# Kernel tuning notes

Measured on AMD Instinct MI355X. Metric: run time of the kernel, lower is better.

## Reference

```python
import jax, jax.numpy as jnp
import numpy as np

D_MODEL = 512
NUM_HEADS = 8
D_FF = 2048
SEQ = 2048
BATCH = 2
EPS = 1e-5


def _linear(x, W, b):
    # x: [S,B,D_in], W: [D_out, D_in] (torch convention), b: [D_out]
    return jnp.einsum('sbd,ed->sbe', x, W) + b


def _layer_norm(x, g, b):
    mu = jnp.mean(x, axis=-1, keepdims=True)
    var = jnp.var(x, axis=-1, keepdims=True)
    return (x - mu) * jax.lax.rsqrt(var + EPS) * g + b


def _mha(q_in, k_in, v_in, W, b, mask4d, num_heads):
    # q_in: [Sq,B,D], k_in/v_in: [Sk,B,D]; W: [4,D,D], b: [4,D]
    Sq, B, D = q_in.shape
    Sk = k_in.shape[0]
    dk = D // num_heads
    q = _linear(q_in, W[0], b[0]).reshape(Sq, B, num_heads, dk).transpose(1, 2, 0, 3)
    k = _linear(k_in, W[1], b[1]).reshape(Sk, B, num_heads, dk).transpose(1, 2, 0, 3)
    v = _linear(v_in, W[2], b[2]).reshape(Sk, B, num_heads, dk).transpose(1, 2, 0, 3)
    scores = jnp.einsum('bhqd,bhkd->bhqk', q, k) / jnp.sqrt(jnp.asarray(dk, q.dtype))
    scores = jnp.where(mask4d, -jnp.inf, scores)
    p = jax.nn.softmax(scores, axis=-1)  # dropout p=0 -> identity
    o = jnp.einsum('bhqk,bhkd->bhqd', p, v)  # [B,H,Sq,dk]
    o = o.transpose(2, 0, 1, 3).reshape(Sq, B, D)
    return _linear(o, W[3], b[3])


def setup_inputs() -> dict:
    key = jax.random.key(0)
    ks = jax.random.split(key, 12)
    scale = 1.0 / np.sqrt(D_MODEL)
    inp = {
        'x': jax.random.normal(ks[0], (SEQ, BATCH, D_MODEL), jnp.float32),
        'memory': jax.random.normal(ks[1], (SEQ, BATCH, D_MODEL), jnp.float32),
        # causal mask: True = masked (strictly upper triangular)
        'tgt_mask': jnp.triu(jnp.ones((SEQ, SEQ), dtype=bool), k=1),
        # per-batch key padding mask for cross attention
        'memory_mask': jax.random.randint(ks[2], (BATCH, SEQ), 0, 2) > 0,
        'sa_W': jax.random.normal(ks[3], (4, D_MODEL, D_MODEL), jnp.float32) * scale,
        'sa_b': jnp.zeros((4, D_MODEL), jnp.float32),
        'ca_W': jax.random.normal(ks[4], (4, D_MODEL, D_MODEL), jnp.float32) * scale,
        'ca_b': jnp.zeros((4, D_MODEL), jnp.float32),
        'w1': jax.random.normal(ks[5], (D_FF, D_MODEL), jnp.float32) * scale,
        'b1': jnp.zeros((D_FF,), jnp.float32),
        'w2': jax.random.normal(ks[6], (D_MODEL, D_FF), jnp.float32) * (1.0 / np.sqrt(D_FF)),
        'b2': jnp.zeros((D_MODEL,), jnp.float32),
        'ln_g': jnp.ones((3, D_MODEL), jnp.float32),
        'ln_b': jnp.zeros((3, D_MODEL), jnp.float32),
    }
    return inp


def reference(x, memory, tgt_mask, memory_mask, sa_W, sa_b, ca_W, ca_b,
              w1, b1, w2, b2, ln_g, ln_b):
    # self-attention block (pre-norm, residual)
    nx = _layer_norm(x, ln_g[0], ln_b[0])
    sa = _mha(nx, nx, nx, sa_W, sa_b, tgt_mask[None, None], NUM_HEADS)
    x = x + sa
    # cross-attention block
    nx = _layer_norm(x, ln_g[1], ln_b[1])
    ca = _mha(nx, memory, memory, ca_W, ca_b, memory_mask[:, None, None, :], NUM_HEADS)
    x = x + ca
    # FFN block
    nx = _layer_norm(x, ln_g[2], ln_b[2])
    ff = _linear(jax.nn.relu(_linear(nx, w1, b1)), w2, b2)
    return x + ff
```

## Files before the change

kernel.cpp:

```cpp
#include <hip/hip_runtime.h>

#define S_LEN 2048
#define BATCH_N 2
#define DM 512
#define H_N 8
#define DK_N 64
#define FF_N 2048
#define M_TOK (S_LEN*BATCH_N)
#define QSZ (BATCH_N*H_N*S_LEN*DK_N)

typedef __attribute__((ext_vector_type(8))) short short8;
typedef __attribute__((ext_vector_type(4))) float f32x4;
typedef __attribute__((ext_vector_type(16))) float f32x16;
typedef __attribute__((ext_vector_type(4))) unsigned uint4v;

__device__ __forceinline__ unsigned short f2b(float f) {
  union { float f; unsigned u; } v; v.f = f;
  unsigned r = v.u + 0x7FFFu + ((v.u >> 16) & 1u);
  return (unsigned short)(r >> 16);
}
__device__ __forceinline__ float b2f(unsigned short u) {
  union { unsigned u; float f; } v; v.u = ((unsigned)u) << 16; return v.f;
}

__device__ __forceinline__ void gl_lds16(const void* g, void* l) {
  __builtin_amdgcn_global_load_lds(
      (__attribute__((address_space(1))) unsigned int*)(unsigned long long)g,
      (__attribute__((address_space(3))) unsigned int*)(unsigned int)(unsigned long long)l,
      16, 0, 0);
}

__global__ void cast_kernel(const float* __restrict__ src,
                            unsigned short* __restrict__ dst, int n) {
  int i = (blockIdx.x * blockDim.x + threadIdx.x) * 4;
  if (i >= n) return;
  float4 v = *(const float4*)(src + i);
  ushort4 o; o.x = f2b(v.x); o.y = f2b(v.y); o.z = f2b(v.z); o.w = f2b(v.w);
  *(ushort4*)(dst + i) = o;
}

__global__ void maskpack(const int* __restrict__ mm, unsigned long long* __restrict__ bm) {
  int t = threadIdx.x;
  int b = t >> 5, kt = t & 31;
  unsigned long long m = 0ull;
  for (int j = 0; j < 64; j++)
    m |= (unsigned long long)(mm[b*S_LEN + kt*64 + j] != 0) << j;
  bm[b*32 + kt] = m;
}

__global__ __launch_bounds__(128) void ln_kernel(const float* __restrict__ in,
                                                 const float* __restrict__ g,
                                                 const float* __restrict__ b,
                                                 unsigned short* __restrict__ out) {
  int row = blockIdx.x, t = threadIdx.x;
  float4 v = ((const float4*)(in + (size_t)row * DM))[t];
  float s  = v.x + v.y + v.z + v.w;
  float ss = v.x*v.x + v.y*v.y + v.z*v.z + v.w*v.w;
  #pragma unroll
  for (int off = 32; off >= 1; off >>= 1) {
    s  += __shfl_xor(s,  off);
    ss += __shfl_xor(ss, off);
  }
  __shared__ float sh[4];
  if ((t & 63) == 0) { sh[(t>>6)*2] = s; sh[(t>>6)*2+1] = ss; }
  __syncthreads();
  s = sh[0] + sh[2]; ss = sh[1] + sh[3];
  float mean = s * (1.f/512.f);
  float inv  = rsqrtf(ss * (1.f/512.f) - mean*mean + 1e-5f);
  float4 gv = ((const float4*)g)[t];
  float4 bv = ((const float4*)b)[t];
  ushort4 o;
  o.x = f2b((v.x-mean)*inv*gv.x + bv.x);
  o.y = f2b((v.y-mean)*inv*gv.y + bv.y);
  o.z = f2b((v.z-mean)*inv*gv.z + bv.z);
  o.w = f2b((v.w-mean)*inv*gv.w + bv.w);
  ((ushort4*)out)[(size_t)row*128 + t] = o;
}

template<int RELU, int OUTMODE, int RESID>
__global__ __launch_bounds__(256) void gemm_bt(
    const unsigned short* __restrict__ A, const unsigned short* __restrict__ W,
    const float* __restrict__ bias, const float* __restrict__ resid,
    float* __restrict__ Cf, unsigned short* __restrict__ Cb,
    int M, int N, int K)
{
  __shared__ unsigned short As[64*40];
  __shared__ unsigned short Bs[64*40];
  int tid = threadIdx.x;
  int lane = tid & 63, w = tid >> 6;
  int wr = w >> 1, wc = w & 1;
  int bm = blockIdx.y * 64, bn = blockIdx.x * 64;
  f32x4 acc[2][2] = {};
  int lrow = tid >> 2;
  int lcg  = (tid & 3) * 8;
  const size_t aoff = (size_t)(bm + lrow) * K + lcg;
  const size_t boff = (size_t)(bn + lrow) * K + lcg;
  int fr = lane & 15, kg = (lane >> 4) * 8;
  short8 pa = *(const short8*)&A[aoff];
  short8 pb = *(const short8*)&W[boff];
  for (int k0 = 0; k0 < K; k0 += 32) {
    *(short8*)&As[lrow*40 + lcg] = pa;
    *(short8*)&Bs[lrow*40 + lcg] = pb;
    if (k0 + 32 < K) {
      pa = *(const short8*)&A[aoff + k0 + 32];
      pb = *(const short8*)&W[boff + k0 + 32];
    }
    __syncthreads();
    short8 af0 = *(const short8*)&As[(wr*32 +      fr)*40 + kg];
    short8 af1 = *(const short8*)&As[(wr*32 + 16 + fr)*40 + kg];
    short8 bf0 = *(const short8*)&Bs[(wc*32 +      fr)*40 + kg];
    short8 bf1 = *(const short8*)&Bs[(wc*32 + 16 + fr)*40 + kg];
    acc[0][0] = __builtin_amdgcn_mfma_f32_16x16x32_bf16(af0, bf0, acc[0][0], 0,0,0);
    acc[0][1] = __builtin_amdgcn_mfma_f32_16x16x32_bf16(af0, bf1, acc[0][1], 0,0,0);
    acc[1][0] = __builtin_amdgcn_mfma_f32_16x16x32_bf16(af1, bf0, acc[1][0], 0,0,0);
    acc[1][1] = __builtin_amdgcn_mfma_f32_16x16x32_bf16(af1, bf1, acc[1][1], 0,0,0);
    __syncthreads();
  }
  int rbase = (lane >> 4) * 4;
  #pragma unroll
  for (int m = 0; m < 2; m++) {
    #pragma unroll
    for (int n = 0; n < 2; n++) {
      int col = bn + wc*32 + n*16 + (lane & 15);
      float bc = bias[col];
      #pragma unroll
      for (int r = 0; r < 4; r++) {
        int row = bm + wr*32 + m*16 + rbase + r;
        float vv = acc[m][n][r] + bc;
        if (RELU) vv = fmaxf(vv, 0.f);
        if (OUTMODE == 2) {
          int which = col >> 9, hh = (col >> 6) & 7, dd = col & 63;
          size_t idx = ((((size_t)which*BATCH_N + (row & 1))*H_N + hh)*S_LEN + (row >> 1))*DK_N + dd;
          Cb[idx] = f2b(vv);
        } else {
          size_t idx = (size_t)row * N + col;
          if (RESID) vv += resid[idx];
          if (OUTMODE == 1) Cb[idx] = f2b(vv);
          else              Cf[idx] = vv;
        }
      }
    }
  }
}

template<int RELU, int OUTMODE, int VSTART>
__global__ __launch_bounds__(256) void gemm128(
    const unsigned short* __restrict__ A, const unsigned short* __restrict__ W,
    const float* __restrict__ bias, unsigned short* __restrict__ Cb,
    int M, int N, int K)
{
  __shared__ unsigned short As[128*32];
  __shared__ unsigned short Bs[128*32];
  int tid = threadIdx.x, lane = tid & 63, w = tid >> 6;
  int bm = blockIdx.y * 128, bn = blockIdx.x * 128;
  int fr = lane & 15, hi = lane >> 4;
  int kg8 = hi*8, rg = hi*4;
  int wm = (w >> 1) * 64, wn = (w & 1) * 64;
  f32x4 acc[4][4] = {};
  const unsigned short* ga0 = A + (size_t)(bm +      (tid>>2))*K + (tid&3)*8;
  const unsigned short* ga1 = A + (size_t)(bm + 64 + (tid>>2))*K + (tid&3)*8;
  const unsigned short* gb0 = W + (size_t)(bn +      (tid>>2))*K + (tid&3)*8;
  const unsigned short* gb1 = W + (size_t)(bn + 64 + (tid>>2))*K + (tid&3)*8;
  unsigned short* lA0 = &As[tid*8];
  unsigned short* lA1 = &As[2048 + tid*8];
  unsigned short* lB0 = &Bs[tid*8];
  unsigned short* lB1 = &Bs[2048 + tid*8];
  for (int k0 = 0; k0 < K; k0 += 32) {
    gl_lds16(ga0 + k0, lA0);
    gl_lds16(ga1 + k0, lA1);
    gl_lds16(gb0 + k0, lB0);
    gl_lds16(gb1 + k0, lB1);
    __syncthreads();
    short8 af[4], bf[4];
    #pragma unroll
    for (int m = 0; m < 4; m++) af[m] = *(const short8*)&As[(wm + m*16 + fr)*32 + kg8];
    #pragma unroll
    for (int n = 0; n < 4; n++) bf[n] = *(const short8*)&Bs[(wn + n*16 + fr)*32 + kg8];
    __builtin_amdgcn_s_setprio(1);
    #pragma unroll
    for (int m = 0; m < 4; m++)
      #pragma unroll
      for (int n = 0; n < 4; n++)
        acc[m][n] = __builtin_amdgcn_mfma_f32_16x16x32_bf16(af[m], bf[n], acc[m][n], 0,0,0);
    __builtin_amdgcn_s_setprio(0);
    __syncthreads();
  }
  #pragma unroll
  for (int m = 0; m < 4; m++) {
    #pragma unroll
    for (int n = 0; n < 4; n++) {
      int col = bn + wn + n*16 + fr;
      float bc = bias[col];
      #pragma unroll
      for (int r = 0; r < 4; r++) {
        int row = bm + wm + m*16 + rg + r;
        float vv = acc[m][n][r] + bc;
        if (RELU) vv = fmaxf(vv, 0.f);
        if (OUTMODE == 2) {
          int which = col >> 9, hh = (col >> 6) & 7, dd = col & 63;
          int srow = row >> 1, bb = row & 1;
          size_t idx;
          if (which >= VSTART)
            idx = (size_t)which*QSZ + (((size_t)bb*H_N + hh)*DK_N + dd)*S_LEN + srow;
          else
            idx = (size_t)which*QSZ + (((size_t)bb*H_N + hh)*S_LEN + srow)*DK_N + dd;
          Cb[idx] = f2b(vv);
        } else {
          Cb[(size_t)row * N + col] = f2b(vv);
        }
      }
    }
  }
}

template<int MODE>
__global__ __launch_bounds__(256, 4) void attn2(
    const unsigned short* __restrict__ qg, const unsigned short* __restrict__ kpl,
    const unsigned short* __restrict__ vtpl, const unsigned long long* __restrict__ bm,
    unsigned short* __restrict__ opart, float* __restrict__ lpart)
{
  __shared__ unsigned short SM[2*64*72 + 128];
  unsigned short* Ks = SM;
  unsigned short* Vt = SM + 64*72;
  float* lsum = (float*)(SM + 2*64*72);
  int tid = threadIdx.x;
  int lane = tid & 63, w = tid >> 6;
  int qgp = w & 1, kh2 = w >> 1;
  int l31 = lane & 31, hi5 = lane >> 5;
  int bid = blockIdx.x;
  int p = bid & 15, u = bid >> 4;
  int qt = u >> 2, range = u & 3;
  int h = p & 7, b = p >> 3;
  const size_t sbase = (size_t)(b*H_N + h) * S_LEN;
  int kt0 = range*8, kt1 = kt0 + 7;
  if (MODE == 0) {
    if (kt0 > qt) {
      int zr = tid >> 2, zc = (tid & 3) * 16;
      short8 z = {};
      size_t zb = (size_t)range*QSZ + (sbase + (size_t)qt*64 + zr)*DK_N + zc;
      *(short8*)&opart[zb]     = z;
      *(short8*)&opart[zb + 8] = z;
      if (tid < 64) lpart[range*32768 + (int)sbase + qt*64 + tid] = 0.f;
      return;
    }
    if (kt1 > qt) kt1 = qt;
  }
  int qrow = qt*64 + qgp*32 + l31;
  short8 qf[4];
  #pragma unroll
  for (int km = 0; km < 4; km++)
    qf[km] = *(const short8*)&qg[(sbase + qrow)*DK_N + km*16 + hi5*8];

  f32x16 oa0 = {}, oa1 = {};
  float lp = 0.f;
  for (int kt = kt0; kt <= kt1; kt++) {
    __syncthreads();
    {
      int sr = tid >> 2, sc = (tid & 3) * 16;
      const unsigned short* kg = &kpl[(sbase + (size_t)kt*64 + sr)*DK_N + sc];
      *(short8*)&Ks[sr*72 + sc]     = *(const short8*)kg;
      *(short8*)&Ks[sr*72 + sc + 8] = *(const short8*)(kg + 8);
      const unsigned short* vg = &vtpl[((size_t)(b*H_N + h)*DK_N + sr)*S_LEN + kt*64 + sc];
      *(short8*)&Vt[sr*72 + sc]     = *(const short8*)vg;
      *(short8*)&Vt[sr*72 + sc + 8] = *(const short8*)(vg + 8);
    }
    __syncthreads();
    f32x16 sa = {};
    __builtin_amdgcn_s_setprio(1);
    #pragma unroll
    for (int km = 0; km < 4; km++) {
      short8 kf = *(const short8*)&Ks[(kh2*32 + l31)*72 + km*16 + hi5*8];
      sa = __builtin_amdgcn_mfma_f32_32x32x16_bf16(kf, qf[km], sa, 0, 0, 0);
    }
    __builtin_amdgcn_s_setprio(0);
    unsigned mlo = 0;
    if (MODE == 1) {
      unsigned long long mw = bm[b*32 + kt];
      mlo = (unsigned)(mw >> (kh2*32 + 4*hi5));
    }
    float pv[16];
    float psum = 0.f;
    int qv = qgp*32 + l31;
    #pragma unroll
    for (int r = 0; r < 16; r++) {
      const int pos = (r & 3) + 8*(r >> 2);
      float e = __expf(sa[r] * 0.125f);
      bool dead;
      if (MODE == 0) dead = (kt == qt) && (kh2*32 + 4*hi5 + pos > qv);
      else           dead = ((mlo >> pos) & 1u) != 0u;
      e = dead ? 0.f : e;
      pv[r] = e;
      psum += e;
    }
    lp += psum;
    unsigned pk[8];
    #pragma unroll
    for (int i = 0; i < 8; i++)
      asm("v_cvt_pk_bf16_f32 %0, %1, %2" : "=v"(pk[i]) : "v"(pv[2*i]), "v"(pv[2*i+1]));
    asm("v_permlane32_swap_b32 %0, %1" : "+v"(pk[0]), "+v"(pk[2]));
    asm("v_permlane32_swap_b32 %0, %1" : "+v"(pk[1]), "+v"(pk[3]));
    asm("v_permlane32_swap_b32 %0, %1" : "+v"(pk[4]), "+v"(pk[6]));
    asm("v_permlane32_swap_b32 %0, %1" : "+v"(pk[5]), "+v"(pk[7]));
    uint4v f0v, f1v;
    f0v.x = pk[0]; f0v.y = pk[1]; f0v.z = pk[2]; f0v.w = pk[3];
    f1v.x = pk[4]; f1v.y = pk[5]; f1v.z = pk[6]; f1v.w = pk[7];
    short8 pf0 = *(short8*)&f0v;
    short8 pf1 = *(short8*)&f1v;
    __builtin_amdgcn_s_setprio(1);
    {
      short8 v00 = *(const short8*)&Vt[(     l31)*72 + kh2*32 +      hi5*8];
      short8 v01 = *(const short8*)&Vt[(     l31)*72 + kh2*32 + 16 + hi5*8];
      oa0 = __builtin_amdgcn_mfma_f32_32x32x16_bf16(pf0, v00, oa0, 0, 0, 0);
      oa0 = __builtin_amdgcn_mfma_f32_32x32x16_bf16(pf1, v01, oa0, 0, 0, 0);
      short8 v10 = *(const short8*)&Vt[(32 + l31)*72 + kh2*32 +      hi5*8];
      short8 v11 = *(const short8*)&Vt[(32 + l31)*72 + kh2*32 + 16 + hi5*8];
      oa1 = __builtin_amdgcn_mfma_f32_32x32x16_bf16(pf0, v10, oa1, 0, 0, 0);
      oa1 = __builtin_amdgcn_mfma_f32_32x32x16_bf16(pf1, v11, oa1, 0, 0, 0);
    }
    __builtin_amdgcn_s_setprio(0);
  }
  float lptot = lp + __shfl_xor(lp, 32);
  float* fb = (float*)SM;
  __syncthreads();
  if (kh2 == 1) {
    #pragma unroll
    for (int r = 0; r < 16; r++) {
      const int pos = (r & 3) + 8*(r >> 2);
      int qr = qgp*32 + pos + 4*hi5;
      fb[qr*64 + l31]      = oa0[r];
      fb[qr*64 + 32 + l31] = oa1[r];
    }
    if (lane < 32) lsum[qgp*32 + l31] = lptot;
  }
  __syncthreads();
  if (kh2 == 0) {
    if (lane < 32)
      lpart[range*32768 + (int)sbase + qt*64 + qgp*32 + l31] = lptot + lsum[qgp*32 + l31];
    #pragma unroll
    for (int r = 0; r < 16; r++) {
      const int pos = (r & 3) + 8*(r >> 2);
      int qr = qgp*32 + pos + 4*hi5;
      size_t obase = (size_t)range*QSZ + (sbase + (size_t)qt*64 + qr)*DK_N;
      opart[obase + l31]      = f2b(oa0[r] + fb[qr*64 + l31]);
      opart[obase + 32 + l31] = f2b(oa1[r] + fb[qr*64 + 32 + l31]);
    }
  }
}

__global__ __launch_bounds__(256) void attn_combine4(
    const unsigned short* __restrict__ op, const float* __restrict__ lp,
    unsigned short* __restrict__ o)
{
  int t = blockIdx.x*256 + threadIdx.x;
  int f = t*8;
  int col = f & 511, row = f >> 9;
  int h = col >> 6, d = col & 63, s = row >> 1, b = row & 1;
  size_t pr = ((size_t)b*H_N + h)*S_LEN + s;
  size_t base = pr*DK_N + d;
  float acc[8] = {0.f,0.f,0.f,0.f,0.f,0.f,0.f,0.f};
  float l = 0.f;
  #pragma unroll
  for (int r = 0; r < 4; r++) {
    short8 a = *(const short8*)&op[(size_t)r*QSZ + base];
    #pragma unroll
    for (int i = 0; i < 8; i++) acc[i] += b2f((unsigned short)a[i]);
    l += lp[r*32768 + (int)pr];
  }
  float inv = 1.f / l;
  short8 r8;
  #pragma unroll
  for (int i = 0; i < 8; i++) r8[i] = (short)f2b(acc[i] * inv);
  *(short8*)&o[(size_t)row*DM + col] = r8;
}

extern "C" void kernel_launch(void* const* d_in, const int* in_sizes, int n_in,
                              void* d_out, int out_size, void* d_ws, size_t ws_size,
                              hipStream_t stream) {
  const float* x       = (const float*)d_in[0];
  const float* memory  = (const float*)d_in[1];
  const int*   memmask = (const int*)d_in[3];
  const float* sa_W = (const float*)d_in[4];
  const float* sa_b = (const float*)d_in[5];
  const float* ca_W = (const float*)d_in[6];
  const float* ca_b = (const float*)d_in[7];
  const float* w1   = (const float*)d_in[8];
  const float* b1   = (const float*)d_in[9];
  const float* w2   = (const float*)d_in[10];
  const float* b2   = (const float*)d_in[11];
  const float* ln_g = (const float*)d_in[12];
  const float* ln_b = (const float*)d_in[13];
  float* out = (float*)d_out;

  char* ws = (char*)d_ws;
  float*          xcur   = (float*)ws;
  unsigned short* nx_bf  = (unsigned short*)(ws + (8u<<20));
  unsigned short* qkv_sa = (unsigned short*)(ws + (12u<<20));
  unsigned short* q_ca   = (unsigned short*)(ws + (24u<<20));
  unsigned short* kv_ca  = (unsigned short*)(ws + (28u<<20));
  unsigned short* o_bf   = (unsigned short*)(ws + (36u<<20));
  unsigned short* mem_bf = (unsigned short*)(ws + (40u<<20));
  unsigned short* h_bf   = (unsigned short*)(ws + (44u<<20));
  unsigned short* opart  = (unsigned short*)(ws + (44u<<20));
  float*          lpart  = (float*)(ws + (60u<<20));
  unsigned long long* bmsk = (unsigned long long*)(ws + (60u<<20) + (1u<<19));
  unsigned short* w_sa   = (unsigned short*)(ws + (61u<<20));
  unsigned short* w_ca   = w_sa + 4*512*512;
  unsigned short* w_f1   = w_ca + 4*512*512;
  unsigned short* w_f2   = w_f1 + 2048*512;

  cast_kernel<<<1024, 256, 0, stream>>>(sa_W, w_sa, 4*512*512);
  cast_kernel<<<1024, 256, 0, stream>>>(ca_W, w_ca, 4*512*512);
  cast_kernel<<<1024, 256, 0, stream>>>(w1,   w_f1, 2048*512);
  cast_kernel<<<1024, 256, 0, stream>>>(w2,   w_f2, 512*2048);
  cast_kernel<<<2048, 256, 0, stream>>>(memory, mem_bf, M_TOK*512);
  maskpack<<<1, 64, 0, stream>>>(memmask, bmsk);

  dim3 blk(256);
  dim3 g512 (512/64,  4096/64);
  dim3 q128_1536(1536/128, 4096/128);
  dim3 q128_1024(1024/128, 4096/128);
  dim3 q128_2048(2048/128, 4096/128);

  ln_kernel<<<4096, 128, 0, stream>>>(x, ln_g, ln_b, nx_bf);
  gemm128<0,2,2><<<q128_1536, blk, 0, stream>>>(nx_bf, w_sa, sa_b, qkv_sa, 4096, 1536, 512);
  attn2<0><<<2048, 256, 0, stream>>>(qkv_sa, qkv_sa + QSZ, qkv_sa + 2*QSZ, nullptr, opart, lpart);
  attn_combine4<<<1024, 256, 0, stream>>>(opart, lpart, o_bf);
  gemm_bt<0,0,1><<<g512, blk, 0, stream>>>(o_bf, w_sa + 3*262144, sa_b + 1536, x, xcur, nullptr, 4096, 512, 512);

  ln_kernel<<<4096, 128, 0, stream>>>(xcur, ln_g + 512, ln_b + 512, nx_bf);
  gemm_bt<0,2,0><<<g512, blk, 0, stream>>>(nx_bf, w_ca, ca_b, nullptr, nullptr, q_ca, 4096, 512, 512);
  gemm128<0,2,1><<<q128_1024, blk, 0, stream>>>(mem_bf, w_ca + 262144, ca_b + 512, kv_ca, 4096, 1024, 512);
  attn2<1><<<2048, 256, 0, stream>>>(q_ca, kv_ca, kv_ca + QSZ, bmsk, opart, lpart);
  attn_combine4<<<1024, 256, 0, stream>>>(opart, lpart, o_bf);
  gemm_bt<0,0,1><<<g512, blk, 0, stream>>>(o_bf, w_ca + 3*262144, ca_b + 1536, xcur, xcur, nullptr, 4096, 512, 512);

  ln_kernel<<<4096, 128, 0, stream>>>(xcur, ln_g + 1024, ln_b + 1024, nx_bf);
  gemm128<1,1,0><<<q128_2048, blk, 0, stream>>>(nx_bf, w_f1, b1, h_bf, 4096, 2048, 512);
  gemm_bt<0,0,1><<<g512, blk, 0, stream>>>(h_bf, w_f2, b2, xcur, out, nullptr, 4096, 512, 2048);
}
```

Measured before the change: 212.3 us.

## Double-buffer LDS tiles in GEMM and attention kernels with register prefetch

Both the GEMM and the attention kernel now keep two LDS buffers. The next tile is loaded into registers while MFMA runs on the current buffer, then written to the alternate buffer before a single barrier. This cuts the two barriers per iteration to one and overlaps global loads with compute. In exchange it doubles LDS use, which can reduce occupancy in the attention kernel (about 37KB per block with launch bounds of 4), and it raises register pressure.

```diff
diff --git a/kernel.cpp b/kernel.cpp
--- a/kernel.cpp
+++ b/kernel.cpp
@@ -84,8 +84,8 @@
     float* __restrict__ Cf, unsigned short* __restrict__ Cb,
     int M, int N, int K)
 {
-  __shared__ unsigned short As[64*40];
-  __shared__ unsigned short Bs[64*40];
+  __shared__ unsigned short As[2][64*40];
+  __shared__ unsigned short Bs[2][64*40];
   int tid = threadIdx.x;
   int lane = tid & 63, w = tid >> 6;
   int wr = w >> 1, wc = w & 1;
@@ -98,23 +98,30 @@
   int fr = lane & 15, kg = (lane >> 4) * 8;
   short8 pa = *(const short8*)&A[aoff];
   short8 pb = *(const short8*)&W[boff];
+  *(short8*)&As[0][lrow*40 + lcg] = pa;
+  *(short8*)&Bs[0][lrow*40 + lcg] = pb;
+  __syncthreads();
+  int cur = 0;
   for (int k0 = 0; k0 < K; k0 += 32) {
-    *(short8*)&As[lrow*40 + lcg] = pa;
-    *(short8*)&Bs[lrow*40 + lcg] = pb;
-    if (k0 + 32 < K) {
+    bool hn = (k0 + 32) < K;
+    if (hn) {
       pa = *(const short8*)&A[aoff + k0 + 32];
       pb = *(const short8*)&W[boff + k0 + 32];
     }
-    __syncthreads();
-    short8 af0 = *(const short8*)&As[(wr*32 +      fr)*40 + kg];
-    short8 af1 = *(const short8*)&As[(wr*32 + 16 + fr)*40 + kg];
-    short8 bf0 = *(const short8*)&Bs[(wc*32 +      fr)*40 + kg];
-    short8 bf1 = *(const short8*)&Bs[(wc*32 + 16 + fr)*40 + kg];
+    short8 af0 = *(const short8*)&As[cur][(wr*32 +      fr)*40 + kg];
+    short8 af1 = *(const short8*)&As[cur][(wr*32 + 16 + fr)*40 + kg];
+    short8 bf0 = *(const short8*)&Bs[cur][(wc*32 +      fr)*40 + kg];
+    short8 bf1 = *(const short8*)&Bs[cur][(wc*32 + 16 + fr)*40 + kg];
     acc[0][0] = __builtin_amdgcn_mfma_f32_16x16x32_bf16(af0, bf0, acc[0][0], 0,0,0);
     acc[0][1] = __builtin_amdgcn_mfma_f32_16x16x32_bf16(af0, bf1, acc[0][1], 0,0,0);
     acc[1][0] = __builtin_amdgcn_mfma_f32_16x16x32_bf16(af1, bf0, acc[1][0], 0,0,0);
     acc[1][1] = __builtin_amdgcn_mfma_f32_16x16x32_bf16(af1, bf1, acc[1][1], 0,0,0);
+    if (hn) {
+      *(short8*)&As[cur^1][lrow*40 + lcg] = pa;
+      *(short8*)&Bs[cur^1][lrow*40 + lcg] = pb;
+    }
     __syncthreads();
+    cur ^= 1;
   }
   int rbase = (lane >> 4) * 4;
   #pragma unroll
@@ -219,10 +226,9 @@
     const unsigned short* __restrict__ vtpl, const unsigned long long* __restrict__ bm,
     unsigned short* __restrict__ opart, float* __restrict__ lpart)
 {
-  __shared__ unsigned short SM[2*64*72 + 128];
-  unsigned short* Ks = SM;
-  unsigned short* Vt = SM + 64*72;
-  float* lsum = (float*)(SM + 2*64*72);
+  __shared__ unsigned short SM[4*64*72 + 128];
+  const int K72 = 64*72;
+  float* lsum = (float*)(SM + 4*K72);
   int tid = threadIdx.x;
   int lane = tid & 63, w = tid >> 6;
   int qgp = w & 1, kh2 = w >> 1;
@@ -251,25 +257,40 @@
   for (int km = 0; km < 4; km++)
     qf[km] = *(const short8*)&qg[(sbase + qrow)*DK_N + km*16 + hi5*8];
 
+  int sr = tid >> 2, sc = (tid & 3) * 16;
+  const unsigned short* kbase = &kpl[(sbase + sr)*DK_N + sc];
+  const unsigned short* vbase = &vtpl[((size_t)(b*H_N + h)*DK_N + sr)*S_LEN + sc];
+  {
+    short8 k0v = *(const short8*)(kbase + (size_t)kt0*64*DK_N);
+    short8 k1v = *(const short8*)(kbase + (size_t)kt0*64*DK_N + 8);
+    short8 v0v = *(const short8*)(vbase + kt0*64);
+    short8 v1v = *(const short8*)(vbase + kt0*64 + 8);
+    *(short8*)&SM[sr*72 + sc]            = k0v;
+    *(short8*)&SM[sr*72 + sc + 8]        = k1v;
+    *(short8*)&SM[K72 + sr*72 + sc]      = v0v;
+    *(short8*)&SM[K72 + sr*72 + sc + 8]  = v1v;
+  }
+  __syncthreads();
+
   f32x16 oa0 = {}, oa1 = {};
   float lp = 0.f;
+  int cur = 0;
   for (int kt = kt0; kt <= kt1; kt++) {
-    __syncthreads();
-    {
-      int sr = tid >> 2, sc = (tid & 3) * 16;
-      const unsigned short* kg = &kpl[(sbase + (size_t)kt*64 + sr)*DK_N + sc];
-      *(short8*)&Ks[sr*72 + sc]     = *(const short8*)kg;
-      *(short8*)&Ks[sr*72 + sc + 8] = *(const short8*)(kg + 8);
-      const unsigned short* vg = &vtpl[((size_t)(b*H_N + h)*DK_N + sr)*S_LEN + kt*64 + sc];
-      *(short8*)&Vt[sr*72 + sc]     = *(const short8*)vg;
-      *(short8*)&Vt[sr*72 + sc + 8] = *(const short8*)(vg + 8);
-    }
-    __syncthreads();
+    bool hn = kt < kt1;
+    short8 nk0, nk1, nv0, nv1;
+    if (hn) {
+      nk0 = *(const short8*)(kbase + (size_t)(kt+1)*64*DK_N);
+      nk1 = *(const short8*)(kbase + (size_t)(kt+1)*64*DK_N + 8);
+      nv0 = *(const short8*)(vbase + (kt+1)*64);
+      nv1 = *(const short8*)(vbase + (kt+1)*64 + 8);
+    }
+    unsigned short* Ksc = SM + cur*2*K72;
+    unsigned short* Vtc = Ksc + K72;
     f32x16 sa = {};
     __builtin_amdgcn_s_setprio(1);
     #pragma unroll
     for (int km = 0; km < 4; km++) {
-      short8 kf = *(const short8*)&Ks[(kh2*32 + l31)*72 + km*16 + hi5*8];
+      short8 kf = *(const short8*)&Ksc[(kh2*32 + l31)*72 + km*16 + hi5*8];
       sa = __builtin_amdgcn_mfma_f32_32x32x16_bf16(kf, qf[km], sa, 0, 0, 0);
     }
     __builtin_amdgcn_s_setprio(0);
@@ -308,20 +329,28 @@
     short8 pf1 = *(short8*)&f1v;
     __builtin_amdgcn_s_setprio(1);
     {
-      short8 v00 = *(const short8*)&Vt[(     l31)*72 + kh2*32 +      hi5*8];
-      short8 v01 = *(const short8*)&Vt[(     l31)*72 + kh2*32 + 16 + hi5*8];
+      short8 v00 = *(const short8*)&Vtc[(     l31)*72 + kh2*32 +      hi5*8];
+      short8 v01 = *(const short8*)&Vtc[(     l31)*72 + kh2*32 + 16 + hi5*8];
       oa0 = __builtin_amdgcn_mfma_f32_32x32x16_bf16(pf0, v00, oa0, 0, 0, 0);
       oa0 = __builtin_amdgcn_mfma_f32_32x32x16_bf16(pf1, v01, oa0, 0, 0, 0);
-      short8 v10 = *(const short8*)&Vt[(32 + l31)*72 + kh2*32 +      hi5*8];
-      short8 v11 = *(const short8*)&Vt[(32 + l31)*72 + kh2*32 + 16 + hi5*8];
+      short8 v10 = *(const short8*)&Vtc[(32 + l31)*72 + kh2*32 +      hi5*8];
+      short8 v11 = *(const short8*)&Vtc[(32 + l31)*72 + kh2*32 + 16 + hi5*8];
       oa1 = __builtin_amdgcn_mfma_f32_32x32x16_bf16(pf0, v10, oa1, 0, 0, 0);
       oa1 = __builtin_amdgcn_mfma_f32_32x32x16_bf16(pf1, v11, oa1, 0, 0, 0);
     }
     __builtin_amdgcn_s_setprio(0);
+    if (hn) {
+      unsigned short* Ksn = SM + (cur^1)*2*K72;
+      *(short8*)&Ksn[sr*72 + sc]           = nk0;
+      *(short8*)&Ksn[sr*72 + sc + 8]       = nk1;
+      *(short8*)&Ksn[K72 + sr*72 + sc]     = nv0;
+      *(short8*)&Ksn[K72 + sr*72 + sc + 8] = nv1;
+    }
+    __syncthreads();
+    cur ^= 1;
   }
   float lptot = lp + __shfl_xor(lp, 32);
   float* fb = (float*)SM;
-  __syncthreads();
   if (kh2 == 1) {
     #pragma unroll
     for (int r = 0; r < 16; r++) {
```

Result: slower. 218.2 us (+2.8%).
